# Kernel tuning notes

Measured on AMD Instinct MI355X. Metric: run time of the kernel, lower is better.

## Reference

```python
import jax, jax.numpy as jnp
import numpy as np

EPS = 1e-8  # torch CosineSimilarity default eps


def setup_inputs() -> dict:
    key = jax.random.key(0)
    k1, k2, k3, k4 = jax.random.split(key, 4)
    cur_insts = jax.random.randint(k1, (200, 1024), 0, 50000)          # [S, B] token ids
    W = jax.random.normal(k2, (50000, 300), dtype=jnp.float32)          # embedding table
    train_embs = jax.random.normal(k3, (100000, 300), dtype=jnp.float32)  # pooled train embeddings
    y_train = jax.random.randint(k4, (100000,), 0, 1000)                # train labels
    return {"cur_insts": cur_insts, "W": W, "train_embs": train_embs, "y_train": y_train}


def reference(cur_insts, W, train_embs, y_train):
    # Embed + mean-pool over the sequence axis (dim 0 in the torch code)
    x = W[cur_insts].mean(axis=0)                                   # [B, d]
    # Cosine similarity: x.y / (max(||x||,eps) * max(||y||,eps))
    xn = jnp.maximum(jnp.linalg.norm(x, axis=1, keepdims=True), EPS)        # [B, 1]
    tn = jnp.maximum(jnp.linalg.norm(train_embs, axis=1, keepdims=True), EPS)  # [N, 1]
    sims = (x @ train_embs.T) / (xn * tn.T)                         # [B, N]
    nn_idx = jnp.argmax(sims, axis=1)                               # [B]
    scores = jnp.max(sims, axis=1)                                  # [B]
    y_pred = y_train[nn_idx]                                        # [B]
    return y_pred, scores
```

## Files before the change

kernel.cpp:

```cpp
#include <hip/hip_runtime.h>
#include <hip/hip_bf16.h>
#include <stdint.h>

#define EPS 1e-8f

typedef __attribute__((ext_vector_type(8))) short bf16x8;
typedef __attribute__((ext_vector_type(4))) float f32x4;
typedef unsigned long long u64;
typedef unsigned int u32;

constexpr int SEQ = 200;
constexpr int B_  = 1024;
constexpr int D_  = 300;
constexpr int DP  = 320;
constexpr int NT  = 100000;
constexpr int BM = 128, BN = 128, BK = 64;
constexpr int NSTRIP = 784;
constexpr int NTP = NSTRIP * BN;
constexpr int CAND_MAX = 4096;
#define MARGIN 2e-3f

__device__ __forceinline__ unsigned short f2bf(float f) {
    u32 b = __float_as_uint(f);
    return (unsigned short)((b + 0x7fffu + ((b >> 16) & 1u)) >> 16);
}
__device__ __forceinline__ u32 simkey(float s) {
    u32 b = __float_as_uint(s);
    return (b & 0x80000000u) ? ~b : (b | 0x80000000u);
}
__device__ __forceinline__ float keysim(u32 k) {
    u32 b = (k & 0x80000000u) ? (k & 0x7fffffffu) : ~k;
    return __uint_as_float(b);
}
__device__ __forceinline__ void gload_lds16(const void* g, void* l) {
    __builtin_amdgcn_global_load_lds(
        (const __attribute__((address_space(1))) unsigned int*)g,
        (__attribute__((address_space(3))) unsigned int*)l, 16, 0, 0);
}

__global__ __launch_bounds__(640) void pool_kernel(
    const int* __restrict__ ids, const float* __restrict__ W,
    float* __restrict__ x, unsigned short* __restrict__ xh,
    float* __restrict__ rxn)
{
    const int b = blockIdx.x;
    const int tid = threadIdx.x;
    __shared__ int sid[SEQ];
    __shared__ float part[640];
    for (int s = tid; s < SEQ; s += 640) sid[s] = ids[s * B_ + b];
    __syncthreads();
    const int half = (tid >= 320) ? 1 : 0;
    const int d = tid - half * 320;
    float a0 = 0.f, a1 = 0.f;
    if (d < D_) {
        const int s0 = half * (SEQ / 2);
        #pragma unroll 2
        for (int s = 0; s < SEQ / 2; s += 2) {
            a0 += W[(size_t)sid[s0 + s]     * D_ + d];
            a1 += W[(size_t)sid[s0 + s + 1] * D_ + d];
        }
    }
    part[tid] = a0 + a1;
    __syncthreads();
    float xv = 0.f;
    if (tid < 320) xv = (part[tid] + part[tid + 320]) * (1.0f / SEQ);
    __syncthreads();
    if (tid < 320) part[tid] = (tid < D_) ? xv * xv : 0.f;
    __syncthreads();
    if (tid < 64) {
        float s = 0.f;
        #pragma unroll
        for (int i = 0; i < 5; ++i) s += part[tid + i * 64];
        #pragma unroll
        for (int m = 32; m >= 1; m >>= 1) s += __shfl_xor(s, m, 64);
        if (tid == 0) rxn[b] = 1.0f / fmaxf(sqrtf(s), EPS);
    }
    if (tid < 320) {
        if (tid < D_) {
            x[(size_t)b * D_ + tid] = xv;
            xh[(size_t)b * DP + tid] = f2bf(xv);
        } else {
            xh[(size_t)b * DP + tid] = 0;
        }
    }
}

__global__ __launch_bounds__(256) void tnorm_kernel(
    const float* __restrict__ T, float* __restrict__ rtn,
    unsigned short* __restrict__ Tb)
{
    const int n = blockIdx.x * 4 + (threadIdx.x >> 6);
    const int lane = threadIdx.x & 63;
    if (n >= NTP) return;
    ushort4* tb = (ushort4*)(Tb + (size_t)n * DP);
    if (n >= NT) {
        ushort4 z = {0, 0, 0, 0};
        tb[lane] = z;
        if (lane < 16) tb[64 + lane] = z;
        return;
    }
    const float4* Tr = (const float4*)(T + (size_t)n * D_);
    float4 v = Tr[lane];
    float s = v.x * v.x + v.y * v.y + v.z * v.z + v.w * v.w;
    ushort4 o; o.x = f2bf(v.x); o.y = f2bf(v.y); o.z = f2bf(v.z); o.w = f2bf(v.w);
    tb[lane] = o;
    if (lane < 16) {
        if (lane < 11) {
            float4 w = Tr[64 + lane];
            s += w.x * w.x + w.y * w.y + w.z * w.z + w.w * w.w;
            ushort4 p; p.x = f2bf(w.x); p.y = f2bf(w.y); p.z = f2bf(w.z); p.w = f2bf(w.w);
            tb[64 + lane] = p;
        } else {
            ushort4 z = {0, 0, 0, 0};
            tb[64 + lane] = z;
        }
    }
    #pragma unroll
    for (int m = 32; m >= 1; m >>= 1) s += __shfl_xor(s, m, 64);
    if (lane == 0) rtn[n] = 1.0f / fmaxf(sqrtf(s), EPS);
}

__global__ __launch_bounds__(256, 3) void gemm_hh_kernel(
    const unsigned short* __restrict__ Ah, const unsigned short* __restrict__ Tb,
    const float* __restrict__ rxn, const float* __restrict__ rtn,
    u32* __restrict__ blockmax)
{
    __shared__ unsigned short sA[BM * BK];
    __shared__ unsigned short sB[BN * BK];
    __shared__ u32 sBest[BM];

    const int tid = threadIdx.x;
    const int g = blockIdx.x;
    const int k8 = g & 7;
    const int t = g >> 3;
    const int bMi = t & 7;
    const int strip = ((t >> 3) << 3) | k8;

    const int lane = tid & 63, wid = tid >> 6;
    const int wm = wid >> 1, wn = wid & 1;
    const int quad = lane >> 4, l15 = lane & 15;

    const unsigned short* pA[4];
    const unsigned short* pB[4];
    int ldsoff[4];
    #pragma unroll
    for (int j = 0; j < 4; ++j) {
        int L = (j * 4 + wid) * 64 + lane;
        int r = L >> 3;
        int c = (L & 7) ^ (r & 7);
        ldsoff[j] = (j * 4 + wid) * 1024;
        pA[j] = Ah + (size_t)(bMi * BM + r) * DP + c * 8;
        pB[j] = Tb + (size_t)(strip * BN + r) * DP + c * 8;
    }

    f32x4 acc[4][4] = {};

    for (int kp = 0; kp < DP; kp += BK) {
        #pragma unroll
        for (int j = 0; j < 4; ++j)
            gload_lds16(pA[j] + kp, (char*)sA + ldsoff[j]);
        #pragma unroll
        for (int j = 0; j < 4; ++j)
            gload_lds16(pB[j] + kp, (char*)sB + ldsoff[j]);
        __syncthreads();

        #pragma unroll
        for (int s = 0; s < 2; ++s) {
            bf16x8 fa[4], fb[4];
            #pragma unroll
            for (int f = 0; f < 4; ++f) {
                int ar = wm * 64 + f * 16 + l15;
                int ac = (s * 4 + quad) ^ (ar & 7);
                fa[f] = *(const bf16x8*)&sA[ar * BK + ac * 8];
                int br = wn * 64 + f * 16 + l15;
                int bc = (s * 4 + quad) ^ (br & 7);
                fb[f] = *(const bf16x8*)&sB[br * BK + bc * 8];
            }
            #pragma unroll
            for (int fm = 0; fm < 4; ++fm)
                #pragma unroll
                for (int fn = 0; fn < 4; ++fn)
                    acc[fm][fn] = __builtin_amdgcn_mfma_f32_16x16x32_bf16(
                        fa[fm], fb[fn], acc[fm][fn], 0, 0, 0);
        }
        __syncthreads();
    }

    if (tid < BM) sBest[tid] = 0u;
    __syncthreads();
    float rt[4];
    const int gn0 = strip * BN + wn * 64 + l15;
    #pragma unroll
    for (int fn = 0; fn < 4; ++fn)
        rt[fn] = (gn0 + fn * 16 < NT) ? rtn[gn0 + fn * 16] : 0.f;
    #pragma unroll
    for (int fm = 0; fm < 4; ++fm) {
        #pragma unroll
        for (int r = 0; r < 4; ++r) {
            int rowl = wm * 64 + fm * 16 + quad * 4 + r;
            float rx = rxn[bMi * BM + rowl];
            u32 bk = 0u;
            #pragma unroll
            for (int fn = 0; fn < 4; ++fn) {
                float sim = acc[fm][fn][r] * rx * rt[fn];
                u32 k = simkey(sim);
                bk = (k > bk) ? k : bk;
            }
            #pragma unroll
            for (int m = 1; m < 16; m <<= 1) {
                u32 o = __shfl_xor(bk, m, 64);
                bk = (o > bk) ? o : bk;
            }
            if (l15 == 0) atomicMax(&sBest[rowl], bk);
        }
    }
    __syncthreads();
    if (tid < BM)
        blockmax[(size_t)(bMi * BM + tid) * NSTRIP + strip] = sBest[tid];
}

__global__ __launch_bounds__(256) void scan_kernel(
    const u32* __restrict__ blockmax, u32* __restrict__ cand,
    u32* __restrict__ count)
{
    const int row = blockIdx.x;
    const int t = threadIdx.x;
    const u32* bmr = blockmax + (size_t)row * NSTRIP;
    u32 m = 0u;
    for (int j = t; j < NSTRIP; j += 256) { u32 e = bmr[j]; m = (e > m) ? e : m; }
    #pragma unroll
    for (int msk = 32; msk >= 1; msk >>= 1) {
        u32 o = __shfl_xor(m, msk, 64);
        m = (o > m) ? o : m;
    }
    __shared__ u32 wred[4];
    __shared__ float thr_s;
    if ((t & 63) == 0) wred[t >> 6] = m;
    __syncthreads();
    if (t == 0) {
        u32 gmx = wred[0];
        for (int i = 1; i < 4; ++i) gmx = (wred[i] > gmx) ? wred[i] : gmx;
        thr_s = keysim(gmx) - MARGIN;
    }
    __syncthreads();
    float thr = thr_s;
    for (int j = t; j < NSTRIP; j += 256) {
        if (keysim(bmr[j]) >= thr) {
            u32 p = atomicAdd(count, 1u);
            if (p < CAND_MAX) cand[p] = ((u32)row << 10) | (u32)j;
        }
    }
}

__global__ __launch_bounds__(256) void rescore_kernel(
    const u32* __restrict__ cand, const u32* __restrict__ count,
    const float* __restrict__ x, const float* __restrict__ T,
    const float* __restrict__ rxn, u64* __restrict__ winner)
{
    u32 cnt = *count; if (cnt > CAND_MAX) cnt = CAND_MAX;
    if (blockIdx.x >= cnt) return;
    u32 c = cand[blockIdx.x];
    const int row = c >> 10, strip = c & 1023;
    __shared__ float4 xs4[75];
    const int t = threadIdx.x;
    if (t < 75) xs4[t] = *(const float4*)&x[(size_t)row * D_ + t * 4];
    __syncthreads();
    const float rx = rxn[row];
    const int w = t >> 6, lane = t & 63;
    u64 best = 0ull;
    for (int cc = 0; cc < 32; ++cc) {
        int n = strip * BN + w * 32 + cc;
        if (n >= NT) break;
        const float4* Tr = (const float4*)(T + (size_t)n * D_);
        float4 v = Tr[lane], xv = xs4[lane];
        float dot = v.x * xv.x + v.y * xv.y + v.z * xv.z + v.w * xv.w;
        float tt  = v.x * v.x + v.y * v.y + v.z * v.z + v.w * v.w;
        if (lane < 11) {
            float4 v2 = Tr[lane + 64], x2 = xs4[lane + 64];
            dot += v2.x * x2.x + v2.y * x2.y + v2.z * x2.z + v2.w * x2.w;
            tt  += v2.x * v2.x + v2.y * v2.y + v2.z * v2.z + v2.w * v2.w;
        }
        #pragma unroll
        for (int m = 32; m >= 1; m >>= 1) {
            dot += __shfl_xor(dot, m, 64);
            tt  += __shfl_xor(tt, m, 64);
        }
        float sim = dot * rx / fmaxf(sqrtf(tt), EPS);
        u64 pk = ((u64)simkey(sim) << 32) | (u32)(~n);
        best = (pk > best) ? pk : best;
    }
    if (lane == 0 && best) atomicMax(&winner[row], best);
}

__global__ __launch_bounds__(64) void final_kernel(
    const u64* __restrict__ winner, const float* __restrict__ x,
    const float* __restrict__ T, const int* __restrict__ y_train,
    float* __restrict__ out)
{
    const int b = blockIdx.x;
    const int lane = threadIdx.x;
    int idx = (int)(~(u32)winner[b]);
    if (idx < 0 || idx >= NT) idx = 0;
    double dot = 0.0, nx = 0.0, nt = 0.0;
    for (int d = lane; d < D_; d += 64) {
        double xv = (double)x[(size_t)b * D_ + d];
        double tv = (double)T[(size_t)idx * D_ + d];
        dot += xv * tv; nx += xv * xv; nt += tv * tv;
    }
    #pragma unroll
    for (int m = 32; m >= 1; m >>= 1) {
        dot += __shfl_xor(dot, m, 64);
        nx  += __shfl_xor(nx, m, 64);
        nt  += __shfl_xor(nt, m, 64);
    }
    if (lane == 0) {
        double score = dot / (fmax(sqrt(nx), (double)EPS) * fmax(sqrt(nt), (double)EPS));
        out[b]      = (float)y_train[idx];
        out[B_ + b] = (float)score;
    }
}

extern "C" void kernel_launch(void* const* d_in, const int* in_sizes, int n_in,
                              void* d_out, int out_size, void* d_ws, size_t ws_size,
                              hipStream_t stream)
{
    const int*   ids = (const int*)d_in[0];
    const float* W   = (const float*)d_in[1];
    const float* T   = (const float*)d_in[2];
    const int*   y   = (const int*)d_in[3];

    char* ws = (char*)d_ws;
    size_t off = 0;
    float* x           = (float*)(ws + off);          off += (size_t)B_ * D_ * 4;
    unsigned short* xh = (unsigned short*)(ws + off); off += (size_t)B_ * DP * 2;
    float* rxn         = (float*)(ws + off);          off += (size_t)B_ * 4;
    float* rtn         = (float*)(ws + off);          off += (size_t)NT * 4;
    unsigned short* Tb = (unsigned short*)(ws + off); off += (size_t)NTP * DP * 2;
    u32* blockmax      = (u32*)(ws + off);            off += (size_t)B_ * NSTRIP * 4;
    u32* cand          = (u32*)(ws + off);            off += (size_t)CAND_MAX * 4;
    u64* winner        = (u64*)(ws + off);            off += (size_t)B_ * 8;
    u32* count         = (u32*)(ws + off);            off += 256;

    hipMemsetAsync(winner, 0, (size_t)B_ * 8 + 256, stream);
    pool_kernel<<<B_, 640, 0, stream>>>(ids, W, x, xh, rxn);
    tnorm_kernel<<<NTP / 4, 256, 0, stream>>>(T, rtn, Tb);
    gemm_hh_kernel<<<8 * NSTRIP, 256, 0, stream>>>(xh, Tb, rxn, rtn, blockmax);
    scan_kernel<<<B_, 256, 0, stream>>>(blockmax, cand, count);
    rescore_kernel<<<CAND_MAX, 256, 0, stream>>>(cand, count, x, T, rxn, winner);
    final_kernel<<<B_, 64, 0, stream>>>(winner, x, T, y, (float*)d_out);
}
```

Measured before the change: 397.6 us.

## Fuse prep kernels, enlarge GEMM M-tile, merge scan/rescore/final into one kernel

Pooling and the train-norm/bf16 conversion now run in one launch, with block index selecting the role. The GEMM uses 256-row M tiles with 512 threads, so each B strip is reused across more rows and fewer blocks are launched. Scan, rescore and final scoring are merged into a per-row finalize kernel with a shared-memory candidate list, which removes the memset, the global atomics and three launches. Rescoring is now serialized per row, and candidates beyond 128 strips are dropped.

```diff
diff --git a/kernel.cpp b/kernel.cpp
--- a/kernel.cpp
+++ b/kernel.cpp
@@ -14,10 +14,11 @@
 constexpr int D_  = 300;
 constexpr int DP  = 320;
 constexpr int NT  = 100000;
-constexpr int BM = 128, BN = 128, BK = 64;
+constexpr int BM = 256, BN = 128, BK = 64;
 constexpr int NSTRIP = 784;
 constexpr int NTP = NSTRIP * BN;
-constexpr int CAND_MAX = 4096;
+constexpr int POOL_BLOCKS = B_;
+constexpr int TN_BLOCKS = (NTP + 4) / 5;
 #define MARGIN 2e-3f
 
 __device__ __forceinline__ unsigned short f2bf(float f) {
@@ -38,89 +39,83 @@
         (__attribute__((address_space(3))) unsigned int*)l, 16, 0, 0);
 }
 
-__global__ __launch_bounds__(640) void pool_kernel(
+__global__ __launch_bounds__(320) void prep_kernel(
     const int* __restrict__ ids, const float* __restrict__ W,
+    const float* __restrict__ T,
     float* __restrict__ x, unsigned short* __restrict__ xh,
-    float* __restrict__ rxn)
-{
-    const int b = blockIdx.x;
-    const int tid = threadIdx.x;
-    __shared__ int sid[SEQ];
-    __shared__ float part[640];
-    for (int s = tid; s < SEQ; s += 640) sid[s] = ids[s * B_ + b];
-    __syncthreads();
-    const int half = (tid >= 320) ? 1 : 0;
-    const int d = tid - half * 320;
-    float a0 = 0.f, a1 = 0.f;
-    if (d < D_) {
-        const int s0 = half * (SEQ / 2);
-        #pragma unroll 2
-        for (int s = 0; s < SEQ / 2; s += 2) {
-            a0 += W[(size_t)sid[s0 + s]     * D_ + d];
-            a1 += W[(size_t)sid[s0 + s + 1] * D_ + d];
-        }
-    }
-    part[tid] = a0 + a1;
-    __syncthreads();
-    float xv = 0.f;
-    if (tid < 320) xv = (part[tid] + part[tid + 320]) * (1.0f / SEQ);
-    __syncthreads();
-    if (tid < 320) part[tid] = (tid < D_) ? xv * xv : 0.f;
-    __syncthreads();
-    if (tid < 64) {
-        float s = 0.f;
-        #pragma unroll
-        for (int i = 0; i < 5; ++i) s += part[tid + i * 64];
-        #pragma unroll
-        for (int m = 32; m >= 1; m >>= 1) s += __shfl_xor(s, m, 64);
-        if (tid == 0) rxn[b] = 1.0f / fmaxf(sqrtf(s), EPS);
-    }
-    if (tid < 320) {
-        if (tid < D_) {
-            x[(size_t)b * D_ + tid] = xv;
-            xh[(size_t)b * DP + tid] = f2bf(xv);
-        } else {
-            xh[(size_t)b * DP + tid] = 0;
-        }
-    }
-}
-
-__global__ __launch_bounds__(256) void tnorm_kernel(
-    const float* __restrict__ T, float* __restrict__ rtn,
+    float* __restrict__ rxn, float* __restrict__ rtn,
     unsigned short* __restrict__ Tb)
 {
-    const int n = blockIdx.x * 4 + (threadIdx.x >> 6);
-    const int lane = threadIdx.x & 63;
-    if (n >= NTP) return;
-    ushort4* tb = (ushort4*)(Tb + (size_t)n * DP);
-    if (n >= NT) {
-        ushort4 z = {0, 0, 0, 0};
-        tb[lane] = z;
-        if (lane < 16) tb[64 + lane] = z;
-        return;
-    }
-    const float4* Tr = (const float4*)(T + (size_t)n * D_);
-    float4 v = Tr[lane];
-    float s = v.x * v.x + v.y * v.y + v.z * v.z + v.w * v.w;
-    ushort4 o; o.x = f2bf(v.x); o.y = f2bf(v.y); o.z = f2bf(v.z); o.w = f2bf(v.w);
-    tb[lane] = o;
-    if (lane < 16) {
-        if (lane < 11) {
-            float4 w = Tr[64 + lane];
-            s += w.x * w.x + w.y * w.y + w.z * w.z + w.w * w.w;
-            ushort4 p; p.x = f2bf(w.x); p.y = f2bf(w.y); p.z = f2bf(w.z); p.w = f2bf(w.w);
-            tb[64 + lane] = p;
+    const int tid = threadIdx.x;
+    if (blockIdx.x < POOL_BLOCKS) {
+        const int b = blockIdx.x;
+        __shared__ int sid[SEQ];
+        __shared__ float red[320];
+        for (int s = tid; s < SEQ; s += 320) sid[s] = ids[s * B_ + b];
+        __syncthreads();
+        const int d = tid;
+        float a0 = 0.f, a1 = 0.f, a2 = 0.f, a3 = 0.f;
+        if (d < D_) {
+            #pragma unroll 2
+            for (int s = 0; s < SEQ; s += 4) {
+                a0 += W[(size_t)sid[s]     * D_ + d];
+                a1 += W[(size_t)sid[s + 1] * D_ + d];
+                a2 += W[(size_t)sid[s + 2] * D_ + d];
+                a3 += W[(size_t)sid[s + 3] * D_ + d];
+            }
+        }
+        float xv = ((a0 + a1) + (a2 + a3)) * (1.0f / SEQ);
+        red[d] = (d < D_) ? xv * xv : 0.f;
+        __syncthreads();
+        if (tid < 64) {
+            float s = 0.f;
+            #pragma unroll
+            for (int i = 0; i < 5; ++i) s += red[tid + i * 64];
+            #pragma unroll
+            for (int m = 32; m >= 1; m >>= 1) s += __shfl_xor(s, m, 64);
+            if (tid == 0) rxn[b] = 1.0f / fmaxf(sqrtf(s), EPS);
+        }
+        if (d < D_) {
+            x[(size_t)b * D_ + d] = xv;
+            xh[(size_t)b * DP + d] = f2bf(xv);
         } else {
+            xh[(size_t)b * DP + d] = 0;
+        }
+    } else {
+        const int n = (blockIdx.x - POOL_BLOCKS) * 5 + (tid >> 6);
+        const int lane = tid & 63;
+        if (n >= NTP) return;
+        ushort4* tb = (ushort4*)(Tb + (size_t)n * DP);
+        if (n >= NT) {
             ushort4 z = {0, 0, 0, 0};
-            tb[64 + lane] = z;
-        }
-    }
-    #pragma unroll
-    for (int m = 32; m >= 1; m >>= 1) s += __shfl_xor(s, m, 64);
-    if (lane == 0) rtn[n] = 1.0f / fmaxf(sqrtf(s), EPS);
-}
-
-__global__ __launch_bounds__(256, 3) void gemm_hh_kernel(
+            tb[lane] = z;
+            if (lane < 16) tb[64 + lane] = z;
+            if (lane == 0) rtn[n] = 0.f;
+            return;
+        }
+        const float4* Tr = (const float4*)(T + (size_t)n * D_);
+        float4 v = Tr[lane];
+        float s = v.x * v.x + v.y * v.y + v.z * v.z + v.w * v.w;
+        ushort4 o; o.x = f2bf(v.x); o.y = f2bf(v.y); o.z = f2bf(v.z); o.w = f2bf(v.w);
+        tb[lane] = o;
+        if (lane < 16) {
+            if (lane < 11) {
+                float4 w = Tr[64 + lane];
+                s += w.x * w.x + w.y * w.y + w.z * w.z + w.w * w.w;
+                ushort4 p; p.x = f2bf(w.x); p.y = f2bf(w.y); p.z = f2bf(w.z); p.w = f2bf(w.w);
+                tb[64 + lane] = p;
+            } else {
+                ushort4 z = {0, 0, 0, 0};
+                tb[64 + lane] = z;
+            }
+        }
+        #pragma unroll
+        for (int m = 32; m >= 1; m >>= 1) s += __shfl_xor(s, m, 64);
+        if (lane == 0) rtn[n] = 1.0f / fmaxf(sqrtf(s), EPS);
+    }
+}
+
+__global__ __launch_bounds__(512, 6) void gemm_hh_kernel(
     const unsigned short* __restrict__ Ah, const unsigned short* __restrict__ Tb,
     const float* __restrict__ rxn, const float* __restrict__ rtn,
     u32* __restrict__ blockmax)
@@ -132,24 +127,30 @@
     const int tid = threadIdx.x;
     const int g = blockIdx.x;
     const int k8 = g & 7;
-    const int t = g >> 3;
-    const int bMi = t & 7;
-    const int strip = ((t >> 3) << 3) | k8;
+    const int h = g >> 3;
+    const int bMi = h & 3;
+    const int strip = ((h >> 2) << 3) | k8;
 
     const int lane = tid & 63, wid = tid >> 6;
     const int wm = wid >> 1, wn = wid & 1;
     const int quad = lane >> 4, l15 = lane & 15;
 
     const unsigned short* pA[4];
-    const unsigned short* pB[4];
-    int ldsoff[4];
+    int laA[4];
     #pragma unroll
     for (int j = 0; j < 4; ++j) {
-        int L = (j * 4 + wid) * 64 + lane;
-        int r = L >> 3;
-        int c = (L & 7) ^ (r & 7);
-        ldsoff[j] = (j * 4 + wid) * 1024;
+        int L = (j * 8 + wid) * 64 + lane;
+        int r = L >> 3, c = (L & 7) ^ (r & 7);
+        laA[j] = (j * 8 + wid) * 1024;
         pA[j] = Ah + (size_t)(bMi * BM + r) * DP + c * 8;
+    }
+    const unsigned short* pB[2];
+    int laB[2];
+    #pragma unroll
+    for (int j = 0; j < 2; ++j) {
+        int L = (j * 8 + wid) * 64 + lane;
+        int r = L >> 3, c = (L & 7) ^ (r & 7);
+        laB[j] = (j * 8 + wid) * 1024;
         pB[j] = Tb + (size_t)(strip * BN + r) * DP + c * 8;
     }
 
@@ -158,10 +159,10 @@
     for (int kp = 0; kp < DP; kp += BK) {
         #pragma unroll
         for (int j = 0; j < 4; ++j)
-            gload_lds16(pA[j] + kp, (char*)sA + ldsoff[j]);
-        #pragma unroll
-        for (int j = 0; j < 4; ++j)
-            gload_lds16(pB[j] + kp, (char*)sB + ldsoff[j]);
+            gload_lds16(pA[j] + kp, (char*)sA + laA[j]);
+        #pragma unroll
+        for (int j = 0; j < 2; ++j)
+            gload_lds16(pB[j] + kp, (char*)sB + laB[j]);
         __syncthreads();
 
         #pragma unroll
@@ -219,13 +220,25 @@
         blockmax[(size_t)(bMi * BM + tid) * NSTRIP + strip] = sBest[tid];
 }
 
-__global__ __launch_bounds__(256) void scan_kernel(
-    const u32* __restrict__ blockmax, u32* __restrict__ cand,
-    u32* __restrict__ count)
+__global__ __launch_bounds__(256) void finalize_kernel(
+    const u32* __restrict__ blockmax, const float* __restrict__ x,
+    const float* __restrict__ T, const float* __restrict__ rxn,
+    const int* __restrict__ y_train, float* __restrict__ out)
 {
     const int row = blockIdx.x;
     const int t = threadIdx.x;
+    const int w = t >> 6, lane = t & 63;
     const u32* bmr = blockmax + (size_t)row * NSTRIP;
+
+    __shared__ u32 wred[4];
+    __shared__ float thr_s;
+    __shared__ int qn_s;
+    __shared__ int ql[128];
+    __shared__ float4 xs4[75];
+    __shared__ u64 wbest[4];
+    __shared__ int widx_s;
+
+    if (t == 0) qn_s = 0;
     u32 m = 0u;
     for (int j = t; j < NSTRIP; j += 256) { u32 e = bmr[j]; m = (e > m) ? e : m; }
     #pragma unroll
@@ -233,9 +246,7 @@
         u32 o = __shfl_xor(m, msk, 64);
         m = (o > m) ? o : m;
     }
-    __shared__ u32 wred[4];
-    __shared__ float thr_s;
-    if ((t & 63) == 0) wred[t >> 6] = m;
+    if (lane == 0) wred[w] = m;
     __syncthreads();
     if (t == 0) {
         u32 gmx = wred[0];
@@ -243,80 +254,72 @@
         thr_s = keysim(gmx) - MARGIN;
     }
     __syncthreads();
-    float thr = thr_s;
+    const float thr = thr_s;
     for (int j = t; j < NSTRIP; j += 256) {
         if (keysim(bmr[j]) >= thr) {
-            u32 p = atomicAdd(count, 1u);
-            if (p < CAND_MAX) cand[p] = ((u32)row << 10) | (u32)j;
-        }
-    }
-}
-
-__global__ __launch_bounds__(256) void rescore_kernel(
-    const u32* __restrict__ cand, const u32* __restrict__ count,
-    const float* __restrict__ x, const float* __restrict__ T,
-    const float* __restrict__ rxn, u64* __restrict__ winner)
-{
-    u32 cnt = *count; if (cnt > CAND_MAX) cnt = CAND_MAX;
-    if (blockIdx.x >= cnt) return;
-    u32 c = cand[blockIdx.x];
-    const int row = c >> 10, strip = c & 1023;
-    __shared__ float4 xs4[75];
-    const int t = threadIdx.x;
+            int p = atomicAdd(&qn_s, 1);
+            if (p < 128) ql[p] = j;
+        }
+    }
     if (t < 75) xs4[t] = *(const float4*)&x[(size_t)row * D_ + t * 4];
     __syncthreads();
+
     const float rx = rxn[row];
-    const int w = t >> 6, lane = t & 63;
+    int nq = qn_s; if (nq > 128) nq = 128;
     u64 best = 0ull;
-    for (int cc = 0; cc < 32; ++cc) {
-        int n = strip * BN + w * 32 + cc;
-        if (n >= NT) break;
-        const float4* Tr = (const float4*)(T + (size_t)n * D_);
-        float4 v = Tr[lane], xv = xs4[lane];
-        float dot = v.x * xv.x + v.y * xv.y + v.z * xv.z + v.w * xv.w;
-        float tt  = v.x * v.x + v.y * v.y + v.z * v.z + v.w * v.w;
-        if (lane < 11) {
-            float4 v2 = Tr[lane + 64], x2 = xs4[lane + 64];
-            dot += v2.x * x2.x + v2.y * x2.y + v2.z * x2.z + v2.w * x2.w;
-            tt  += v2.x * v2.x + v2.y * v2.y + v2.z * v2.z + v2.w * v2.w;
-        }
-        #pragma unroll
-        for (int m = 32; m >= 1; m >>= 1) {
-            dot += __shfl_xor(dot, m, 64);
-            tt  += __shfl_xor(tt, m, 64);
-        }
-        float sim = dot * rx / fmaxf(sqrtf(tt), EPS);
-        u64 pk = ((u64)simkey(sim) << 32) | (u32)(~n);
-        best = (pk > best) ? pk : best;
-    }
-    if (lane == 0 && best) atomicMax(&winner[row], best);
-}
-
-__global__ __launch_bounds__(64) void final_kernel(
-    const u64* __restrict__ winner, const float* __restrict__ x,
-    const float* __restrict__ T, const int* __restrict__ y_train,
-    float* __restrict__ out)
-{
-    const int b = blockIdx.x;
-    const int lane = threadIdx.x;
-    int idx = (int)(~(u32)winner[b]);
-    if (idx < 0 || idx >= NT) idx = 0;
-    double dot = 0.0, nx = 0.0, nt = 0.0;
-    for (int d = lane; d < D_; d += 64) {
-        double xv = (double)x[(size_t)b * D_ + d];
-        double tv = (double)T[(size_t)idx * D_ + d];
-        dot += xv * tv; nx += xv * xv; nt += tv * tv;
-    }
-    #pragma unroll
-    for (int m = 32; m >= 1; m >>= 1) {
-        dot += __shfl_xor(dot, m, 64);
-        nx  += __shfl_xor(nx, m, 64);
-        nt  += __shfl_xor(nt, m, 64);
-    }
-    if (lane == 0) {
-        double score = dot / (fmax(sqrt(nx), (double)EPS) * fmax(sqrt(nt), (double)EPS));
-        out[b]      = (float)y_train[idx];
-        out[B_ + b] = (float)score;
+    for (int q = 0; q < nq; ++q) {
+        const int strip = ql[q];
+        for (int cc = 0; cc < 32; ++cc) {
+            int n = strip * BN + w * 32 + cc;
+            if (n >= NT) continue;
+            const float4* Tr = (const float4*)(T + (size_t)n * D_);
+            float4 v = Tr[lane], xv = xs4[lane];
+            float dot = v.x * xv.x + v.y * xv.y + v.z * xv.z + v.w * xv.w;
+            float tt  = v.x * v.x + v.y * v.y + v.z * v.z + v.w * v.w;
+            if (lane < 11) {
+                float4 v2 = Tr[64 + lane], x2 = xs4[64 + lane];
+                dot += v2.x * x2.x + v2.y * x2.y + v2.z * x2.z + v2.w * x2.w;
+                tt  += v2.x * v2.x + v2.y * v2.y + v2.z * v2.z + v2.w * v2.w;
+            }
+            #pragma unroll
+            for (int msk = 32; msk >= 1; msk >>= 1) {
+                dot += __shfl_xor(dot, msk, 64);
+                tt  += __shfl_xor(tt, msk, 64);
+            }
+            float sim = dot * rx / fmaxf(sqrtf(tt), EPS);
+            u64 pk = ((u64)simkey(sim) << 32) | (u32)(~n);
+            best = (pk > best) ? pk : best;
+        }
+    }
+    if (lane == 0) wbest[w] = best;
+    __syncthreads();
+    if (t == 0) {
+        u64 gb = wbest[0];
+        for (int i = 1; i < 4; ++i) gb = (wbest[i] > gb) ? wbest[i] : gb;
+        int idx = (int)(~(u32)gb);
+        if (idx < 0 || idx >= NT) idx = 0;
+        widx_s = idx;
+    }
+    __syncthreads();
+    if (w == 0) {
+        const int idx = widx_s;
+        double dot = 0.0, nx = 0.0, nt = 0.0;
+        for (int d = lane; d < D_; d += 64) {
+            double xv = (double)x[(size_t)row * D_ + d];
+            double tv = (double)T[(size_t)idx * D_ + d];
+            dot += xv * tv; nx += xv * xv; nt += tv * tv;
+        }
+        #pragma unroll
+        for (int msk = 32; msk >= 1; msk >>= 1) {
+            dot += __shfl_xor(dot, msk, 64);
+            nx  += __shfl_xor(nx, msk, 64);
+            nt  += __shfl_xor(nt, msk, 64);
+        }
+        if (lane == 0) {
+            double score = dot / (fmax(sqrt(nx), (double)EPS) * fmax(sqrt(nt), (double)EPS));
+            out[row]      = (float)y_train[idx];
+            out[B_ + row] = (float)score;
+        }
     }
 }
 
@@ -334,18 +337,10 @@
     float* x           = (float*)(ws + off);          off += (size_t)B_ * D_ * 4;
     unsigned short* xh = (unsigned short*)(ws + off); off += (size_t)B_ * DP * 2;
     float* rxn         = (float*)(ws + off);          off += (size_t)B_ * 4;
-    float* rtn         = (float*)(ws + off);          off += (size_t)NT * 4;
+    float* rtn         = (float*)(ws + off);          off += (size_t)NTP * 4;
     unsigned short* Tb = (unsigned short*)(ws + off); off += (size_t)NTP * DP * 2;
     u32* blockmax      = (u32*)(ws + off);            off += (size_t)B_ * NSTRIP * 4;
-    u32* cand          = (u32*)(ws + off);            off += (size_t)CAND_MAX * 4;
-    u64* winner        = (u64*)(ws + off);            off += (size_t)B_ * 8;
-    u32* count         = (u32*)(ws + off);            off += 256;
-
-    hipMemsetAsync(winner, 0, (size_t)B_ * 8 + 256, stream);
-    pool_kernel<<<B_, 640, 0, stream>>>(ids, W, x, xh, rxn);
-    tnorm_kernel<<<NTP / 4, 256, 0, stream>>>(T, rtn, Tb);
-    gemm_hh_kernel<<<8 * NSTRIP, 256, 0, stream>>>(xh, Tb, rxn, rtn, blockmax);
-    scan_kernel<<<B_, 256, 0, stream>>>(blockmax, cand, count);
-    rescore_kernel<<<CAND_MAX, 256, 0, stream>>>(cand, count, x, T, rxn, winner);
-    final_kernel<<<B_, 64, 0, stream>>>(winner, x, T, y, (float*)d_out);
-}
+    prep_kernel<<<POOL_BLOCKS + TN_BLOCKS, 320, 0, stream>>>(ids, W, T, x, xh, rxn, rtn, Tb);
+    gemm_hh_kernel<<<NSTRIP * 4, 512, 0, stream>>>(xh, Tb, rxn, rtn, blockmax);
+    finalize_kernel<<<B_, 256, 0, stream>>>(blockmax, x, T, rxn, y, (float*)d_out);
+}
```

New measurement: 807.0 us. 103% more time.
